# Kernel tuning notes

Hardware: AMD Instinct MI355X
Metric: run time of the kernel (lower is better)

## Reference

```python
import jax, jax.numpy as jnp
import numpy as np

H = 16          # head_count
D = 1024        # model_dim
DPH = D // H    # dim_per_head


def setup_inputs() -> dict:
    key0 = jax.random.key(0)
    ks = jax.random.split(key0, 13)
    B, S = 4, 2048
    scale = 1.0 / np.sqrt(D)
    inp = {
        "key": jax.random.normal(ks[0], (B, S, D), jnp.float32),
        "value": jax.random.normal(ks[1], (B, S, D), jnp.float32),
        "query": jax.random.normal(ks[2], (B, S, D), jnp.float32),
        "mask": jax.random.randint(ks[3], (B, S, S), 0, 2).astype(jnp.bool_),
        "Wq": jax.random.normal(ks[4], (D, D), jnp.float32) * scale,
        "bq": jnp.zeros((D,), jnp.float32),
        "Wk": jax.random.normal(ks[5], (D, D), jnp.float32) * scale,
        "bk": jnp.zeros((D,), jnp.float32),
        "Wv": jax.random.normal(ks[6], (D, D), jnp.float32) * scale,
        "bv": jnp.zeros((D,), jnp.float32),
        "Wo": jax.random.normal(ks[7], (D, D), jnp.float32) * scale,
        "bo": jnp.zeros((D,), jnp.float32),
    }
    return inp


def _shape(x, B):
    # [B, S, D] -> [B, H, S, DPH]
    return x.reshape(B, -1, H, DPH).transpose(0, 2, 1, 3)


def reference(key, value, query, mask, Wq, bq, Wk, bk, Wv, bv, Wo, bo):
    B, S, _ = key.shape
    k_up = _shape(key @ Wk + bk, B)                       # [B,H,S,DPH]
    v_up = _shape(value @ Wv + bv, B)                     # [B,H,S,DPH]
    q_up = _shape(query @ Wq + bq, B) / jnp.sqrt(jnp.asarray(DPH, key.dtype))
    scores = jnp.einsum('bhqd,bhkd->bhqk', q_up, k_up)    # [B,H,S,S]
    scores = jnp.where(mask[:, None, :, :], jnp.asarray(-1e18, scores.dtype), scores)
    attn = jax.nn.softmax(scores, axis=-1)                # dropout = identity (eval)
    context = jnp.einsum('bhqk,bhkd->bhqd', attn, v_up)   # [B,H,S,DPH]
    context = context.transpose(0, 2, 1, 3).reshape(B, S, H * DPH)
    return context @ Wo + bo
```

## Files before the change

kernel.cpp:

```cpp
#include <hip/hip_runtime.h>

typedef _Float16 half8 __attribute__((ext_vector_type(8)));
typedef _Float16 half4 __attribute__((ext_vector_type(4)));
typedef float floatx4 __attribute__((ext_vector_type(4)));
typedef float floatx16 __attribute__((ext_vector_type(16)));

#define MFMA16(A,B,C) __builtin_amdgcn_mfma_f32_16x16x32_f16((A),(B),(C),0,0,0)
#define MFMA32(A,B,C) __builtin_amdgcn_mfma_f32_32x32x16_f16((A),(B),(C),0,0,0)


__global__ __launch_bounds__(256) void maskpack(
    const int* __restrict__ m, unsigned int* __restrict__ p)
{
  const int w = blockIdx.x * 256 + threadIdx.x;
  const int4* s = (const int4*)(m + (size_t)w * 32);
  unsigned int bits = 0;
#pragma unroll
  for (int j = 0; j < 8; ++j) {
    const int4 v = s[j];
    bits |= (v.x ? 1u : 0u) << (j * 4 + 0);
    bits |= (v.y ? 1u : 0u) << (j * 4 + 1);
    bits |= (v.z ? 1u : 0u) << (j * 4 + 2);
    bits |= (v.w ? 1u : 0u) << (j * 4 + 3);
  }
  p[w] = bits;
}

__global__ __launch_bounds__(256) void wconv(
    const float* __restrict__ Wq, const float* __restrict__ Wk,
    const float* __restrict__ Wv, const float* __restrict__ Wo,
    _Float16* __restrict__ dst)
{
  const float* W = (blockIdx.z == 0) ? Wq : (blockIdx.z == 1) ? Wk
                  : (blockIdx.z == 2) ? Wv : Wo;
  _Float16* WT = dst + (size_t)blockIdx.z * 1024 * 1024;
  __shared__ float t[32][33];
  const int tx = threadIdx.x & 31;
  const int ty = threadIdx.x >> 5;
  const int k0 = blockIdx.x * 32, n0 = blockIdx.y * 32;
#pragma unroll
  for (int j = 0; j < 4; ++j)
    t[ty + j * 8][tx] = W[(size_t)(k0 + ty + j * 8) * 1024 + n0 + tx];
  __syncthreads();
#pragma unroll
  for (int j = 0; j < 4; ++j)
    WT[(size_t)(n0 + ty + j * 8) * 1024 + k0 + tx] = (_Float16)t[tx][ty + j * 8];
}

template <int OP>
__global__ __launch_bounds__(256) void gemm_k(
    const void* __restrict__ Ap, const _Float16* __restrict__ BT,
    const float* __restrict__ bias, void* __restrict__ Cp)
{
  __shared__ __align__(16) _Float16 As[128 * 64];
  __shared__ __align__(16) _Float16 Bs[128 * 64];
  const int tid = threadIdx.x;
  const int lane = tid & 63;
  const int wv = tid >> 6;
  const int m0 = blockIdx.x * 128;
  const int n0 = blockIdx.y * 128;
  const int wr = (wv >> 1) * 64;
  const int wc = (wv & 1) * 64;

  floatx4 acc[4][4];
#pragma unroll
  for (int i = 0; i < 4; ++i)
#pragma unroll
    for (int j = 0; j < 4; ++j) acc[i][j] = (floatx4){0.f, 0.f, 0.f, 0.f};

  char* AsB = (char*)As;
  char* BsB = (char*)Bs;

  for (int ko = 0; ko < 1024; ko += 64) {
#pragma unroll
    for (int r = 0; r < 4; ++r) {
      const int idx = (r * 256 + tid) * 8;
      const int row = idx >> 6;
      const int colh = idx & 63;
      const int dstb = row * 128 + ((colh * 2) ^ ((row & 7) << 4));
      if (OP == 3) {
        const _Float16* s = (const _Float16*)Ap + (size_t)(m0 + row) * 1024 + ko + colh;
        *(half8*)(AsB + dstb) = *(const half8*)s;
      } else {
        const float* s = (const float*)Ap + (size_t)(m0 + row) * 1024 + ko + colh;
        floatx4 v0 = *(const floatx4*)s;
        floatx4 v1 = *(const floatx4*)(s + 4);
        half8 hv;
        hv[0] = (_Float16)v0[0]; hv[1] = (_Float16)v0[1];
        hv[2] = (_Float16)v0[2]; hv[3] = (_Float16)v0[3];
        hv[4] = (_Float16)v1[0]; hv[5] = (_Float16)v1[1];
        hv[6] = (_Float16)v1[2]; hv[7] = (_Float16)v1[3];
        *(half8*)(AsB + dstb) = hv;
      }
      const _Float16* bs = BT + (size_t)(n0 + row) * 1024 + ko + colh;
      *(half8*)(BsB + dstb) = *(const half8*)bs;
    }
    __syncthreads();
#pragma unroll
    for (int kk = 0; kk < 64; kk += 32) {
      half8 af[4], bf[4];
#pragma unroll
      for (int mi = 0; mi < 4; ++mi) {
        const int row = wr + mi * 16 + (lane & 15);
        const int cb = (kk + (lane >> 4) * 8) * 2;
        af[mi] = *(const half8*)(AsB + row * 128 + (cb ^ ((row & 7) << 4)));
      }
#pragma unroll
      for (int ni = 0; ni < 4; ++ni) {
        const int row = wc + ni * 16 + (lane & 15);
        const int cb = (kk + (lane >> 4) * 8) * 2;
        bf[ni] = *(const half8*)(BsB + row * 128 + (cb ^ ((row & 7) << 4)));
      }
#pragma unroll
      for (int mi = 0; mi < 4; ++mi)
#pragma unroll
        for (int ni = 0; ni < 4; ++ni)
          acc[mi][ni] = MFMA16(af[mi], bf[ni], acc[mi][ni]);
    }
    __syncthreads();
  }

#pragma unroll
  for (int ni = 0; ni < 4; ++ni) {
    const int nn = n0 + wc + ni * 16 + (lane & 15);
    const float bvv = bias[nn];
#pragma unroll
    for (int mi = 0; mi < 4; ++mi) {
      floatx4 c = acc[mi][ni];
#pragma unroll
      for (int i = 0; i < 4; ++i) {
        const int mm = m0 + wr + mi * 16 + (lane >> 4) * 4 + i;
        float val = c[i] + bvv;
        if (OP == 0) val *= 0.1803368801111204f;
        if (OP == 0 || OP == 1) {
          _Float16* o = (_Float16*)Cp;
          const size_t off =
              ((size_t)((mm >> 11) * 16 + (nn >> 6)) * 2048 + (mm & 2047)) * 64 + (nn & 63);
          o[off] = (_Float16)val;
        } else if (OP == 2) {
          _Float16* o = (_Float16*)Cp;
          const size_t off =
              ((size_t)((mm >> 11) * 16 + (nn >> 6)) * 64 + (nn & 63)) * 2048 + (mm & 2047);
          o[off] = (_Float16)val;
        } else {
          float* o = (float*)Cp;
          o[(size_t)mm * 1024 + nn] = val;
        }
      }
    }
  }
}

__global__ __launch_bounds__(256) void attn_k(
    const _Float16* __restrict__ q_up, const _Float16* __restrict__ k_up,
    const _Float16* __restrict__ vT, const unsigned int* __restrict__ pmask,
    _Float16* __restrict__ ctx)
{
  const int tid = threadIdx.x;
  const int lane = tid & 63;
  const int wv = tid >> 6;
  const int bid = blockIdx.x;
  const int xcd = bid & 7;
  const int slot = bid >> 3;
  const int bh = xcd * 8 + (slot & 7);
  const int qc = slot >> 3;
  const int b = bh >> 4;
  const int h = bh & 15;
  const int l31 = lane & 31;
  const int hi = lane >> 5;
  const int qw = qc * 256 + wv * 64;

  const _Float16* qb = q_up + ((size_t)bh * 2048 + qw) * 64;
  const _Float16* kb = k_up + (size_t)bh * 2048 * 64;
  const _Float16* vb = vT + (size_t)bh * 64 * 2048;
  const unsigned int* mroww = pmask + ((size_t)b * 2048 + qw + l31) * 64;

  half8 qf[2][4];
#pragma unroll
  for (int qt = 0; qt < 2; ++qt)
#pragma unroll
    for (int kk = 0; kk < 4; ++kk)
      qf[qt][kk] = *(const half8*)(qb + (size_t)(qt * 32 + l31) * 64 + kk * 16 + hi * 8);

  floatx16 O[2][2];
#pragma unroll
  for (int qt = 0; qt < 2; ++qt)
#pragma unroll
    for (int dt = 0; dt < 2; ++dt)
#pragma unroll
      for (int r = 0; r < 16; ++r) O[qt][dt][r] = 0.f;
  float lsum[2] = {0.f, 0.f};

  half8 kfA[4], kfB[4];
  unsigned int mwA[2], mwB[2];

#define LOADK(KF, MW, K0)                                                      \
  do {                                                                         \
    _Pragma("unroll")                                                          \
    for (int kk = 0; kk < 4; ++kk)                                             \
      KF[kk] = *(const half8*)(kb + (size_t)((K0) + l31) * 64 + kk * 16 + hi * 8); \
    MW[0] = mroww[(K0) >> 5];                                                  \
    MW[1] = mroww[32 * 64 + ((K0) >> 5)];                                      \
  } while (0)

  auto STEP = [&](const half8 (&kf)[4], const unsigned int (&mw)[2], int k0) {
    half8 vf[2][2];
#pragma unroll
    for (int dt = 0; dt < 2; ++dt)
#pragma unroll
      for (int kk2 = 0; kk2 < 2; ++kk2)
        vf[dt][kk2] = *(const half8*)(vb + (size_t)(dt * 32 + l31) * 2048 + k0 + kk2 * 16 + hi * 8);

    floatx16 s[2];
    __builtin_amdgcn_s_setprio(1);
#pragma unroll
    for (int qt = 0; qt < 2; ++qt) {
      floatx16 a;
#pragma unroll
      for (int r = 0; r < 16; ++r) a[r] = 0.f;
      a = MFMA32(kf[0], qf[qt][0], a);
      a = MFMA32(kf[1], qf[qt][1], a);
      a = MFMA32(kf[2], qf[qt][2], a);
      s[qt] = MFMA32(kf[3], qf[qt][3], a);
    }
    __builtin_amdgcn_s_setprio(0);

#pragma unroll
    for (int qt = 0; qt < 2; ++qt) {
      const unsigned int mh = mw[qt] >> (4 * hi);
      float e[16];
#pragma unroll
      for (int m = 0; m < 4; ++m) {
        const unsigned int bm = mh >> (8 * m);
#pragma unroll
        for (int j = 0; j < 4; ++j)
          e[4 * m + j] =
              ((bm >> j) & 1u) ? 0.f : __builtin_amdgcn_exp2f(s[qt][4 * m + j]);
      }
      float u0 = (e[0] + e[1]) + (e[2] + e[3]);
      float u1 = (e[4] + e[5]) + (e[6] + e[7]);
      float u2 = (e[8] + e[9]) + (e[10] + e[11]);
      float u3 = (e[12] + e[13]) + (e[14] + e[15]);
      lsum[qt] += (u0 + u1) + (u2 + u3);

      unsigned int c0 = __builtin_bit_cast(unsigned int, __builtin_amdgcn_cvt_pkrtz(e[0], e[1]));
      unsigned int c1 = __builtin_bit_cast(unsigned int, __builtin_amdgcn_cvt_pkrtz(e[2], e[3]));
      unsigned int c2 = __builtin_bit_cast(unsigned int, __builtin_amdgcn_cvt_pkrtz(e[4], e[5]));
      unsigned int c3 = __builtin_bit_cast(unsigned int, __builtin_amdgcn_cvt_pkrtz(e[6], e[7]));
      unsigned int c4 = __builtin_bit_cast(unsigned int, __builtin_amdgcn_cvt_pkrtz(e[8], e[9]));
      unsigned int c5 = __builtin_bit_cast(unsigned int, __builtin_amdgcn_cvt_pkrtz(e[10], e[11]));
      unsigned int c6 = __builtin_bit_cast(unsigned int, __builtin_amdgcn_cvt_pkrtz(e[12], e[13]));
      unsigned int c7 = __builtin_bit_cast(unsigned int, __builtin_amdgcn_cvt_pkrtz(e[14], e[15]));
      const unsigned int ra = __shfl_xor(hi ? c0 : c2, 32);
      const unsigned int rb = __shfl_xor(hi ? c1 : c3, 32);
      const unsigned int rc = __shfl_xor(hi ? c4 : c6, 32);
      const unsigned int rd = __shfl_xor(hi ? c5 : c7, 32);
      union { half8 v; unsigned int u[4]; } p0, p1;
      p0.u[0] = hi ? ra : c0;  p0.u[1] = hi ? rb : c1;
      p0.u[2] = hi ? c2 : ra;  p0.u[3] = hi ? c3 : rb;
      p1.u[0] = hi ? rc : c4;  p1.u[1] = hi ? rd : c5;
      p1.u[2] = hi ? c6 : rc;  p1.u[3] = hi ? c7 : rd;
      __builtin_amdgcn_s_setprio(1);
#pragma unroll
      for (int dt = 0; dt < 2; ++dt) {
        O[qt][dt] = MFMA32(vf[dt][0], p0.v, O[qt][dt]);
        O[qt][dt] = MFMA32(vf[dt][1], p1.v, O[qt][dt]);
      }
      __builtin_amdgcn_s_setprio(0);
    }
  };

  LOADK(kfA, mwA, 0);
#pragma unroll 1
  for (int k0 = 0; k0 < 2048; k0 += 64) {
    LOADK(kfB, mwB, k0 + 32);
    STEP(kfA, mwA, k0);
    LOADK(kfA, mwA, (k0 + 64) & 2047);
    STEP(kfB, mwB, k0 + 32);
  }
#undef LOADK

#pragma unroll
  for (int qt = 0; qt < 2; ++qt) {
    const float tot = lsum[qt] + __shfl_xor(lsum[qt], 32);
    const float inv = 1.f / tot;
    const size_t rowb = ((size_t)(b * 2048 + qw + qt * 32 + l31)) * 1024 + h * 64;
#pragma unroll
    for (int dt = 0; dt < 2; ++dt) {
#pragma unroll
      for (int m = 0; m < 4; ++m) {
        half4 w4;
        w4[0] = (_Float16)(O[qt][dt][4 * m + 0] * inv);
        w4[1] = (_Float16)(O[qt][dt][4 * m + 1] * inv);
        w4[2] = (_Float16)(O[qt][dt][4 * m + 2] * inv);
        w4[3] = (_Float16)(O[qt][dt][4 * m + 3] * inv);
        *(half4*)(ctx + rowb + dt * 32 + 8 * m + 4 * hi) = w4;
      }
    }
  }
}

extern "C" void kernel_launch(void* const* d_in, const int* in_sizes, int n_in,
                              void* d_out, int out_size, void* d_ws, size_t ws_size,
                              hipStream_t stream) {
  const float* key   = (const float*)d_in[0];
  const float* value = (const float*)d_in[1];
  const float* query = (const float*)d_in[2];
  const int*   mask  = (const int*)d_in[3];
  const float* Wq = (const float*)d_in[4];
  const float* bq = (const float*)d_in[5];
  const float* Wk = (const float*)d_in[6];
  const float* bk = (const float*)d_in[7];
  const float* Wv = (const float*)d_in[8];
  const float* bv = (const float*)d_in[9];
  const float* Wo = (const float*)d_in[10];
  const float* bo = (const float*)d_in[11];

  _Float16* wsp = (_Float16*)d_ws;
  _Float16* WT   = wsp;
  _Float16* q_up = wsp + (size_t)4 * 1024 * 1024;
  _Float16* k_up = q_up + (size_t)8192 * 1024;
  _Float16* vT   = k_up + (size_t)8192 * 1024;
  _Float16* ctx  = vT + (size_t)8192 * 1024;
  unsigned int* pmask = (unsigned int*)(ctx + (size_t)8192 * 1024);

  maskpack<<<dim3(2048), 256, 0, stream>>>(mask, pmask);
  wconv<<<dim3(32, 32, 4), 256, 0, stream>>>(Wq, Wk, Wv, Wo, WT);
  gemm_k<0><<<dim3(64, 8), 256, 0, stream>>>(query, WT, bq, q_up);
  gemm_k<1><<<dim3(64, 8), 256, 0, stream>>>(key, WT + (size_t)1024 * 1024, bk, k_up);
  gemm_k<2><<<dim3(64, 8), 256, 0, stream>>>(value, WT + (size_t)2 * 1024 * 1024, bv, vT);
  attn_k<<<dim3(512), 256, 0, stream>>>(q_up, k_up, vT, pmask, ctx);
  gemm_k<3><<<dim3(64, 8), 256, 0, stream>>>(ctx, WT + (size_t)3 * 1024 * 1024, bo, (float*)d_out);
}
```

Before: 303.4 us.

## Stage K/V tiles through swizzled shared memory and transpose packed mask

The attention kernel now loads each 32-key K tile and V tile cooperatively into double-buffered, XOR-swizzled LDS, so the four waves of a block share one global load instead of each wave fetching the same K/V separately. Register prefetch of the next tile overlaps with compute, and a barrier follows each step. The packed mask is written transposed so per-tile mask words for consecutive query rows are contiguous, which coalesces mask reads. This trades per-wave global traffic for LDS traffic plus a __syncthreads per tile.

```diff
diff --git a/kernel.cpp b/kernel.cpp
--- a/kernel.cpp
+++ b/kernel.cpp
@@ -13,17 +13,21 @@
     const int* __restrict__ m, unsigned int* __restrict__ p)
 {
   const int w = blockIdx.x * 256 + threadIdx.x;
-  const int4* s = (const int4*)(m + (size_t)w * 32);
+  const int b = w >> 17;
+  const int rem = w & 131071;
+  const int s = rem >> 6;
+  const int wp = rem & 63;
+  const int4* src = (const int4*)(m + (size_t)w * 32);
   unsigned int bits = 0;
 #pragma unroll
   for (int j = 0; j < 8; ++j) {
-    const int4 v = s[j];
+    const int4 v = src[j];
     bits |= (v.x ? 1u : 0u) << (j * 4 + 0);
     bits |= (v.y ? 1u : 0u) << (j * 4 + 1);
     bits |= (v.z ? 1u : 0u) << (j * 4 + 2);
     bits |= (v.w ? 1u : 0u) << (j * 4 + 3);
   }
-  p[w] = bits;
+  p[((size_t)(b * 64 + wp)) * 2048 + s] = bits;
 }
 
 __global__ __launch_bounds__(256) void wconv(
@@ -153,7 +157,7 @@
 
 __global__ __launch_bounds__(256) void attn_k(
     const _Float16* __restrict__ q_up, const _Float16* __restrict__ k_up,
-    const _Float16* __restrict__ vT, const unsigned int* __restrict__ pmask,
+    const _Float16* __restrict__ vT, const unsigned int* __restrict__ pmaskT,
     _Float16* __restrict__ ctx)
 {
   const int tid = threadIdx.x;
@@ -170,10 +174,22 @@
   const int hi = lane >> 5;
   const int qw = qc * 256 + wv * 64;
 
+  __shared__ __align__(16) _Float16 Kl[2][32 * 64];
+  __shared__ __align__(16) _Float16 Vl[2][64 * 32];
+
   const _Float16* qb = q_up + ((size_t)bh * 2048 + qw) * 64;
   const _Float16* kb = k_up + (size_t)bh * 2048 * 64;
   const _Float16* vb = vT + (size_t)bh * 64 * 2048;
-  const unsigned int* mroww = pmask + ((size_t)b * 2048 + qw + l31) * 64;
+  const unsigned int* mbase = pmaskT + (size_t)(b * 64) * 2048 + qw + l31;
+
+  const int krow = tid >> 3, kseg = tid & 7;
+  const int kByte = krow * 128 + ((kseg * 16) ^ ((krow & 7) << 4));
+  const int vrow = tid >> 2, vseg = tid & 3;
+  const int vByte = vrow * 64 + ((vseg * 16) ^ ((vrow & 3) << 4));
+  const _Float16* gK = kb + tid * 8;
+  const _Float16* gV = vb + (size_t)vrow * 2048 + vseg * 8;
+  char* KB = (char*)Kl;
+  char* VB = (char*)Vl;
 
   half8 qf[2][4];
 #pragma unroll
@@ -191,25 +207,24 @@
       for (int r = 0; r < 16; ++r) O[qt][dt][r] = 0.f;
   float lsum[2] = {0.f, 0.f};
 
-  half8 kfA[4], kfB[4];
-  unsigned int mwA[2], mwB[2];
-
-#define LOADK(KF, MW, K0)                                                      \
-  do {                                                                         \
-    _Pragma("unroll")                                                          \
-    for (int kk = 0; kk < 4; ++kk)                                             \
-      KF[kk] = *(const half8*)(kb + (size_t)((K0) + l31) * 64 + kk * 16 + hi * 8); \
-    MW[0] = mroww[(K0) >> 5];                                                  \
-    MW[1] = mroww[32 * 64 + ((K0) >> 5)];                                      \
-  } while (0)
-
-  auto STEP = [&](const half8 (&kf)[4], const unsigned int (&mw)[2], int k0) {
+  half8 stK, stV;
+
+  auto COMPUTE = [&](int buf, int t) {
+    unsigned int mw[2];
+    mw[0] = mbase[(size_t)t * 2048];
+    mw[1] = mbase[(size_t)t * 2048 + 32];
+    half8 kf[4];
+#pragma unroll
+    for (int kk = 0; kk < 4; ++kk)
+      kf[kk] = *(const half8*)(KB + buf * 4096 + l31 * 128 +
+                               ((kk * 32 + hi * 16) ^ ((l31 & 7) << 4)));
     half8 vf[2][2];
 #pragma unroll
     for (int dt = 0; dt < 2; ++dt)
 #pragma unroll
       for (int kk2 = 0; kk2 < 2; ++kk2)
-        vf[dt][kk2] = *(const half8*)(vb + (size_t)(dt * 32 + l31) * 2048 + k0 + kk2 * 16 + hi * 8);
+        vf[dt][kk2] = *(const half8*)(VB + buf * 4096 + (dt * 32 + l31) * 64 +
+                                      ((kk2 * 32 + hi * 16) ^ ((l31 & 3) << 4)));
 
     floatx16 s[2];
     __builtin_amdgcn_s_setprio(1);
@@ -270,15 +285,35 @@
     }
   };
 
-  LOADK(kfA, mwA, 0);
+  stK = *(const half8*)gK;
+  stV = *(const half8*)gV;
+  *(half8*)(KB + kByte) = stK;
+  *(half8*)(VB + vByte) = stV;
+  stK = *(const half8*)(gK + 2048);
+  stV = *(const half8*)(gV + 32);
+  __syncthreads();
+
 #pragma unroll 1
-  for (int k0 = 0; k0 < 2048; k0 += 64) {
-    LOADK(kfB, mwB, k0 + 32);
-    STEP(kfA, mwA, k0);
-    LOADK(kfA, mwA, (k0 + 64) & 2047);
-    STEP(kfB, mwB, k0 + 32);
-  }
-#undef LOADK
+  for (int t = 0; t < 64; t += 2) {
+    {
+      *(half8*)(KB + 4096 + kByte) = stK;
+      *(half8*)(VB + 4096 + vByte) = stV;
+      const int tn = (t + 2 < 64) ? t + 2 : 0;
+      stK = *(const half8*)(gK + (size_t)tn * 2048);
+      stV = *(const half8*)(gV + tn * 32);
+      COMPUTE(0, t);
+      __syncthreads();
+    }
+    {
+      *(half8*)(KB + kByte) = stK;
+      *(half8*)(VB + vByte) = stV;
+      const int tn = (t + 3 < 64) ? t + 3 : 0;
+      stK = *(const half8*)(gK + (size_t)tn * 2048);
+      stV = *(const half8*)(gV + tn * 32);
+      COMPUTE(1, t + 1);
+      __syncthreads();
+    }
+  }
 
 #pragma unroll
   for (int qt = 0; qt < 2; ++qt) {
@@ -322,13 +357,13 @@
   _Float16* k_up = q_up + (size_t)8192 * 1024;
   _Float16* vT   = k_up + (size_t)8192 * 1024;
   _Float16* ctx  = vT + (size_t)8192 * 1024;
-  unsigned int* pmask = (unsigned int*)(ctx + (size_t)8192 * 1024);
-
-  maskpack<<<dim3(2048), 256, 0, stream>>>(mask, pmask);
+  unsigned int* pmaskT = (unsigned int*)(ctx + (size_t)8192 * 1024);
+
+  maskpack<<<dim3(2048), 256, 0, stream>>>(mask, pmaskT);
   wconv<<<dim3(32, 32, 4), 256, 0, stream>>>(Wq, Wk, Wv, Wo, WT);
   gemm_k<0><<<dim3(64, 8), 256, 0, stream>>>(query, WT, bq, q_up);
   gemm_k<1><<<dim3(64, 8), 256, 0, stream>>>(key, WT + (size_t)1024 * 1024, bk, k_up);
   gemm_k<2><<<dim3(64, 8), 256, 0, stream>>>(value, WT + (size_t)2 * 1024 * 1024, bv, vT);
-  attn_k<<<dim3(512), 256, 0, stream>>>(q_up, k_up, vT, pmask, ctx);
+  attn_k<<<dim3(512), 256, 0, stream>>>(q_up, k_up, vT, pmaskT, ctx);
   gemm_k<3><<<dim3(64, 8), 256, 0, stream>>>(ctx, WT + (size_t)3 * 1024 * 1024, bo, (float*)d_out);
 }
```

Result: faster. 289.7 us (-4.5%).
